# Kernel optimization log

Hardware: AMD Instinct MI355X
Metric: run time of the kernel (lower is better)

Reference implementation:

```python
import jax, jax.numpy as jnp
import numpy as np

HIDDEN = 1024
NUM_HEAD = 16
HEAD_DIM = HIDDEN // NUM_HEAD


def setup_inputs() -> dict:
    key = jax.random.key(0)
    ks = jax.random.split(key, 12)
    bs, seq = 4, 2048
    inp = {
        'srcQ': jax.random.normal(ks[0], (bs, seq, HIDDEN), jnp.float32),
        'srcK': jax.random.normal(ks[1], (bs, seq, HIDDEN), jnp.float32),
        'srcV': jax.random.normal(ks[2], (bs, seq, HIDDEN), jnp.float32),
        'mask': jnp.ones((bs, 1, 1, seq), jnp.int32),
        'Wq': jax.random.normal(ks[3], (HIDDEN, HIDDEN), jnp.float32) * 0.02,
        'bq': jnp.zeros((HIDDEN,), jnp.float32),
        'Wk': jax.random.normal(ks[4], (HIDDEN, HIDDEN), jnp.float32) * 0.02,
        'bk': jnp.zeros((HIDDEN,), jnp.float32),
        'Wv': jax.random.normal(ks[5], (HIDDEN, HIDDEN), jnp.float32) * 0.02,
        'bv': jnp.zeros((HIDDEN,), jnp.float32),
        'Wo': jax.random.normal(ks[6], (HIDDEN, HIDDEN), jnp.float32) * 0.02,
        'bo': jnp.zeros((HIDDEN,), jnp.float32),
    }
    return inp


def _split_heads(x):
    # [bs, seq, hidden] -> [bs, num_head, seq, head_dim]
    bs, seq, _ = x.shape
    return x.reshape(bs, seq, NUM_HEAD, HEAD_DIM).transpose(0, 2, 1, 3)


def reference(srcQ, srcK, srcV, mask, Wq, bq, Wk, bk, Wv, bv, Wo, bo):
    Q = _split_heads(srcQ @ Wq + bq)
    K = _split_heads(srcK @ Wk + bk)
    V = _split_heads(srcV @ Wv + bv)
    # NOTE: original module applies NO 1/sqrt(d) scaling (scale tensor unused)
    scores = jnp.einsum('bhqd,bhkd->bhqk', Q, K)
    scores = jnp.where(mask == 0, jnp.float32(-10000.0), scores)
    attn = jax.nn.softmax(scores, axis=-1)  # dropout is identity in eval
    out = jnp.einsum('bhqk,bhkd->bhqd', attn, V)
    bs, _, seq, _ = out.shape
    out = out.transpose(0, 2, 1, 3).reshape(bs, seq, HIDDEN)
    return out @ Wo + bo
```

## Files before the change

### kernel.cpp

```cpp
#include <hip/hip_runtime.h>

typedef short bf16x8 __attribute__((ext_vector_type(8)));
typedef short bf16x4 __attribute__((ext_vector_type(4)));
typedef float f32x4 __attribute__((ext_vector_type(4)));
typedef unsigned short ushort8 __attribute__((ext_vector_type(8)));
typedef unsigned short ushort4v __attribute__((ext_vector_type(4)));
typedef unsigned int uint4v __attribute__((ext_vector_type(4)));
typedef float float4v __attribute__((ext_vector_type(4)));

#define LOG2E 1.4426950408889634f
#define MASKED_VAL -14426.950408889634f

__device__ __forceinline__ unsigned short f2bf(float f) {
  unsigned u = __builtin_bit_cast(unsigned, f);
  u = u + 0x7fffu + ((u >> 16) & 1u);
  return (unsigned short)(u >> 16);
}

__device__ __forceinline__ unsigned pk2(float a, float b) {
  unsigned r;
  asm("v_cvt_pk_bf16_f32 %0, %1, %2" : "=v"(r) : "v"(a), "v"(b));
  return r;
}

__device__ __forceinline__ float exp2a(float x) {
  float r;
  asm("v_exp_f32 %0, %1" : "=v"(r) : "v"(x));
  return r;
}

__device__ __forceinline__ void gload16(const void* g, void* l) {
  __builtin_amdgcn_global_load_lds(
      (const __attribute__((address_space(1))) unsigned int*)g,
      (__attribute__((address_space(3))) unsigned int*)l, 16, 0, 0);
}

__global__ __launch_bounds__(256) void pack_w4(const float* __restrict__ W0,
                                               const float* __restrict__ W1,
                                               const float* __restrict__ W2,
                                               const float* __restrict__ W3,
                                               unsigned short* __restrict__ P) {
  __shared__ float tile[32][33];
  const int z = blockIdx.z;
  const float* W = (z == 0) ? W0 : (z == 1) ? W1 : (z == 2) ? W2 : W3;
  unsigned short* o = P + (size_t)z * (1 << 20);
  int bx = blockIdx.x * 32;
  int by = blockIdx.y * 32;
  int tx = threadIdx.x & 31;
  int ty = threadIdx.x >> 5;
#pragma unroll
  for (int j = 0; j < 32; j += 8)
    tile[ty + j][tx] = W[(size_t)(by + ty + j) * 1024 + bx + tx];
  __syncthreads();
  const int t = threadIdx.x;
  if (t < 128) {
    int col_l = t & 31, kg = t >> 5;
    int col = bx + col_l;
    ushort8 v;
#pragma unroll
    for (int j = 0; j < 8; ++j) v[j] = f2bf(tile[kg * 8 + j][col_l]);
    int bn = col >> 7, cl = col & 127;
    int wc = cl >> 6, n = (cl >> 4) & 3, lr = cl & 15;
    int ks = by >> 5;
    size_t off = (size_t)(bn * 32 + ks) * 4096 + (wc * 4 + n) * 512 + (kg * 16 + lr) * 8;
    *(ushort8*)&o[off] = v;
  }
}

__global__ __launch_bounds__(256, 3) void gemm_qkv(
    const float* __restrict__ srcQ, const float* __restrict__ srcK,
    const float* __restrict__ srcV, const unsigned short* __restrict__ Wp,
    const float* __restrict__ bq, const float* __restrict__ bk,
    const float* __restrict__ bv, unsigned short* __restrict__ Qb,
    unsigned short* __restrict__ Kb, unsigned short* __restrict__ Vt) {
  __shared__ __align__(16) unsigned short As[3][128 * 32];
  const int K = 1024, N = 1024;
  const int chunk = blockIdx.x >> 9;
  const int inner = blockIdx.x & 511;
  const int x = inner & 7, i = inner >> 3;
  const int bm = (x << 3) + (i >> 3);
  const int bn = i & 7;
  const float* Af = (chunk == 0) ? srcQ : (chunk == 1) ? srcK : srcV;
  const unsigned short* Pk = Wp + (size_t)chunk * (1 << 20);
  const float* bias = (chunk == 0) ? bq : (chunk == 1) ? bk : bv;
  const float scale = (chunk == 0) ? LOG2E : 1.0f;
  const int t = threadIdx.x;
  const int lane = t & 63, wid = t >> 6;
  const int wr = wid >> 1, wc = wid & 1;
  const int lr = lane & 15, lg = lane >> 4;
  f32x4 acc[4][4] = {};
  const size_t baseA = (size_t)(bm * 128) * K;
  const int c0 = t, c1 = t + 256;
  const size_t a0off = baseA + (size_t)(c0 >> 2) * K + (c0 & 3) * 8;
  const size_t a1off = baseA + (size_t)(c1 >> 2) * K + (c1 & 3) * 8;
  size_t bo[4];
#pragma unroll
  for (int n = 0; n < 4; ++n)
    bo[n] = (size_t)(bn * 32) * 4096 + (size_t)(wc * 4 + n) * 512 + (size_t)lane * 8;

  unsigned short* pA0 = &As[0][0];
  unsigned short* pA1 = &As[1][0];
  unsigned short* pA2 = &As[2][0];
  float4v fE[4], fO[4];
  bf16x8 bE[4], bO[4];

  auto loadA = [&](float4v* f, int ke) {
    f[0] = *(const float4v*)&Af[a0off + ke];
    f[1] = *(const float4v*)&Af[a0off + ke + 4];
    f[2] = *(const float4v*)&Af[a1off + ke];
    f[3] = *(const float4v*)&Af[a1off + ke + 4];
  };
  auto loadB = [&](bf16x8* b, int ks) {
#pragma unroll
    for (int n = 0; n < 4; ++n)
      b[n] = *(const bf16x8*)&Pk[bo[n] + (size_t)ks * 4096];
  };
  auto writeA = [&](const float4v* f, unsigned short* dst) {
    uint4v w0, w1;
    w0[0] = pk2(f[0][0], f[0][1]); w0[1] = pk2(f[0][2], f[0][3]);
    w0[2] = pk2(f[1][0], f[1][1]); w0[3] = pk2(f[1][2], f[1][3]);
    w1[0] = pk2(f[2][0], f[2][1]); w1[1] = pk2(f[2][2], f[2][3]);
    w1[2] = pk2(f[3][0], f[3][1]); w1[3] = pk2(f[3][2], f[3][3]);
    *(uint4v*)&dst[c0 * 8] = w0;
    *(uint4v*)&dst[c1 * 8] = w1;
  };
  auto compute = [&](const bf16x8* b) {
    bf16x8 a[4];
#pragma unroll
    for (int m = 0; m < 4; ++m)
      a[m] = *(const bf16x8*)&pA0[(wr * 64 + 16 * m + lr) * 32 + lg * 8];
    __builtin_amdgcn_s_setprio(1);
#pragma unroll
    for (int m = 0; m < 4; ++m)
#pragma unroll
      for (int n = 0; n < 4; ++n)
        acc[m][n] = __builtin_amdgcn_mfma_f32_16x16x32_bf16(a[m], b[n], acc[m][n], 0, 0, 0);
    __builtin_amdgcn_s_setprio(0);
  };
  auto rotate = [&]() {
    unsigned short* ta = pA0; pA0 = pA1; pA1 = pA2; pA2 = ta;
  };

  loadA(fE, 0);
  loadB(bE, 0);
  loadA(fO, 32);
  loadB(bO, 1);
  writeA(fE, pA0);
  asm volatile("s_waitcnt lgkmcnt(0)" ::: "memory");
  __builtin_amdgcn_s_barrier();

  for (int it = 0; it < 16; ++it) {
    const int t0 = 2 * it;
    if (it < 15) loadA(fE, 32 * (t0 + 2));
    compute(bE);
    if (t0 + 2 < 32) loadB(bE, t0 + 2);
    writeA(fO, pA1);
    asm volatile("s_waitcnt lgkmcnt(0)" ::: "memory");
    __builtin_amdgcn_sched_barrier(0);
    __builtin_amdgcn_s_barrier();
    rotate();
    if (it < 15) loadA(fO, 32 * (t0 + 3));
    compute(bO);
    if (t0 + 3 < 32) loadB(bO, t0 + 3);
    if (it < 15) {
      writeA(fE, pA1);
      asm volatile("s_waitcnt lgkmcnt(0)" ::: "memory");
      __builtin_amdgcn_sched_barrier(0);
      __builtin_amdgcn_s_barrier();
      rotate();
    }
  }

  const int rowb = bm * 128 + wr * 64;
  const int colb = bn * 128 + wc * 64;
  if (chunk == 2) {
    const int bidx = rowb >> 11;
    const int srow = rowb & 2047;
#pragma unroll
    for (int n = 0; n < 4; ++n) {
      int col = colb + 16 * n + lr;
      float bv_ = bias[col];
#pragma unroll
      for (int m = 0; m < 4; ++m) {
        int s0 = srow + 16 * m + 4 * lg;
        ushort4v u;
#pragma unroll
        for (int r = 0; r < 4; ++r) u[r] = f2bf(acc[m][n][r] + bv_);
        *(ushort4v*)&Vt[((size_t)(bidx * 1024 + col)) * 2048 + s0] = u;
      }
    }
  } else {
    unsigned short* C = (chunk == 0) ? Qb : Kb;
#pragma unroll
    for (int n = 0; n < 4; ++n) {
      int col = colb + 16 * n + lr;
      float bv_ = bias[col];
#pragma unroll
      for (int m = 0; m < 4; ++m) {
        int row0 = rowb + 16 * m + 4 * lg;
#pragma unroll
        for (int r = 0; r < 4; ++r)
          C[(size_t)(row0 + r) * N + col] = f2bf((acc[m][n][r] + bv_) * scale);
      }
    }
  }
}

__global__ __launch_bounds__(256, 3) void gemm_out(const unsigned short* __restrict__ A,
                                                   const unsigned short* __restrict__ Bp,
                                                   const float* __restrict__ bias,
                                                   float* __restrict__ C) {
  __shared__ __align__(16) unsigned short As[3][128 * 32];
  const int K = 1024, N = 1024;
  const int x = blockIdx.x & 7, i = blockIdx.x >> 3;
  const int bm = (x << 3) + (i >> 3);
  const int bn = i & 7;
  const int t = threadIdx.x;
  const int lane = t & 63, wid = t >> 6;
  const int wr = wid >> 1, wc = wid & 1;
  const int lr = lane & 15, lg = lane >> 4;
  f32x4 acc[4][4] = {};
  const size_t baseA = (size_t)(bm * 128) * K;
  const int c0 = t, c1 = t + 256;
  const size_t a0off = baseA + (size_t)(c0 >> 2) * K + (c0 & 3) * 8;
  const size_t a1off = baseA + (size_t)(c1 >> 2) * K + (c1 & 3) * 8;
  size_t bo[4];
#pragma unroll
  for (int n = 0; n < 4; ++n)
    bo[n] = (size_t)(bn * 32) * 4096 + (size_t)(wc * 4 + n) * 512 + (size_t)lane * 8;

  unsigned short* pA0 = &As[0][0];
  unsigned short* pA1 = &As[1][0];
  unsigned short* pA2 = &As[2][0];
  bf16x8 bE[4], bO[4];

  auto dmaA = [&](int ks, unsigned short* dA) {
    gload16(&A[a0off + 32 * ks], &dA[c0 * 8]);
    gload16(&A[a1off + 32 * ks], &dA[c1 * 8]);
  };
  auto loadB = [&](bf16x8* b, int ks) {
#pragma unroll
    for (int n = 0; n < 4; ++n)
      b[n] = *(const bf16x8*)&Bp[bo[n] + (size_t)ks * 4096];
  };
  auto compute = [&](const bf16x8* b) {
    bf16x8 a[4];
#pragma unroll
    for (int m = 0; m < 4; ++m)
      a[m] = *(const bf16x8*)&pA0[(wr * 64 + 16 * m + lr) * 32 + lg * 8];
    __builtin_amdgcn_s_setprio(1);
#pragma unroll
    for (int m = 0; m < 4; ++m)
#pragma unroll
      for (int n = 0; n < 4; ++n)
        acc[m][n] = __builtin_amdgcn_mfma_f32_16x16x32_bf16(a[m], b[n], acc[m][n], 0, 0, 0);
    __builtin_amdgcn_s_setprio(0);
  };
  auto rotate = [&]() {
    unsigned short* ta = pA0; pA0 = pA1; pA1 = pA2; pA2 = ta;
  };

  dmaA(0, pA0);
  dmaA(1, pA1);
  loadB(bE, 0);
  loadB(bO, 1);
  asm volatile("s_waitcnt vmcnt(10)" ::: "memory");
  __builtin_amdgcn_sched_barrier(0);
  __builtin_amdgcn_s_barrier();

  for (int it = 0; it < 16; ++it) {
    const int t0 = 2 * it;
    if (t0 + 2 < 32) dmaA(t0 + 2, pA2);
    compute(bE);
    if (t0 + 2 < 32) loadB(bE, t0 + 2);
    {
      if (t0 < 30) {
        asm volatile("s_waitcnt vmcnt(6)" ::: "memory");
      } else {
        asm volatile("s_waitcnt vmcnt(0)" ::: "memory");
      }
      __builtin_amdgcn_sched_barrier(0);
      __builtin_amdgcn_s_barrier();
      rotate();
    }
    if (t0 + 3 < 32) dmaA(t0 + 3, pA2);
    compute(bO);
    if (t0 + 3 < 32) loadB(bO, t0 + 3);
    if (it < 15) {
      if (t0 + 1 < 30) {
        asm volatile("s_waitcnt vmcnt(6)" ::: "memory");
      } else {
        asm volatile("s_waitcnt vmcnt(0)" ::: "memory");
      }
      __builtin_amdgcn_sched_barrier(0);
      __builtin_amdgcn_s_barrier();
      rotate();
    }
  }

  const int rowb = bm * 128 + wr * 64;
  const int colb = bn * 128 + wc * 64;
#pragma unroll
  for (int n = 0; n < 4; ++n) {
    int col = colb + 16 * n + lr;
    float bv = bias[col];
#pragma unroll
    for (int m = 0; m < 4; ++m) {
      int row0 = rowb + 16 * m + 4 * lg;
#pragma unroll
      for (int r = 0; r < 4; ++r)
        C[(size_t)(row0 + r) * N + col] = acc[m][n][r] + bv;
    }
  }
}

__global__ __launch_bounds__(512, 4) void attn_kernel(
    const unsigned short* __restrict__ Q, const unsigned short* __restrict__ K,
    const unsigned short* __restrict__ V, const int* __restrict__ mask,
    unsigned short* __restrict__ ctx) {
  __shared__ __align__(16) unsigned short pool[16384];
  __shared__ int s_any[8];
  unsigned short* Kbuf0 = pool;
  unsigned short* Kbuf1 = pool + 4096;
  unsigned short* Vbuf0 = pool + 8192;
  unsigned short* Vbuf1 = pool + 12288;
  const int g = blockIdx.x;
  const int bid = (g & 7) * 64 + (g >> 3);
  const int qb = bid & 7, h = (bid >> 3) & 15, b = bid >> 7;
  const int t = threadIdx.x;
  const int lane = t & 63, wid = t >> 6;
  const int lr = lane & 15, lg = lane >> 4;
  const size_t rowQ0 = (size_t)(b * 2048 + qb * 256);
  const int hcol = h * 64;
  const size_t vrow0 = (size_t)((b * 16 + h) * 64) * 2048;

  const int row_s = t >> 3, pos_s = t & 7;
  const size_t ksrc = (size_t)(b * 2048 + row_s) * 1024 + hcol + ((pos_s ^ (row_s & 7)) << 3);
  const size_t vsrc = vrow0 + (size_t)row_s * 2048 + ((pos_s ^ ((row_s >> 1) & 7)) << 3);
  const int ldso = t * 8;

#pragma unroll
  for (int i = 0; i < 4; ++i) {
    int ci = t + 512 * i;
    int row = ci >> 3, pos = ci & 7;
    gload16(&Q[(rowQ0 + row) * 1024 + hcol + ((pos ^ (row & 7)) << 3)], &pool[ci * 8]);
  }
  const int* mb = mask + b * 2048;
  int4 mv0 = *(const int4*)&mb[t * 4];
  int bad = (mv0.x == 0) | (mv0.y == 0) | (mv0.z == 0) | (mv0.w == 0);
  unsigned long long bb = __ballot(bad);
  if (lane == 0) s_any[wid] = (bb != 0ULL);
  __syncthreads();
  bf16x8 aq[2][2];
#pragma unroll
  for (int m = 0; m < 2; ++m)
#pragma unroll
    for (int kd = 0; kd < 2; ++kd) {
      int row = wid * 32 + 16 * m + lr;
      int ch = (4 * kd + lg) ^ (lr & 7);
      aq[m][kd] = *(const bf16x8*)&pool[row * 64 + ch * 8];
    }
  int anyi = 0;
#pragma unroll
  for (int w = 0; w < 8; ++w) anyi |= s_any[w];
  const bool anymask = anyi != 0;
  __syncthreads();
  gload16(&K[ksrc], &Kbuf0[ldso]);
  gload16(&V[vsrc], &Vbuf0[ldso]);
  __syncthreads();

  f32x4 o[2][4] = {};
  f32x4 ol[2] = {};
  const short oneb = 0x3F80;
  const bf16x8 ones8 = {oneb, oneb, oneb, oneb, oneb, oneb, oneb, oneb};
  const f32x4 zero4 = {0.f, 0.f, 0.f, 0.f};
  const int ch0 = (lg ^ (lr & 7)) * 8;
  const int ch1 = ((4 + lg) ^ (lr & 7)) * 8;
  const int sw = lr >> 1;

  for (int kb = 0; kb < 32; ++kb) {
    const int bi = kb & 1;
    const unsigned short* Kb_ = bi ? Kbuf1 : Kbuf0;
    const unsigned short* Vb_ = bi ? Vbuf1 : Vbuf0;
    unsigned short* Kn_ = bi ? Kbuf0 : Kbuf1;
    unsigned short* Vn_ = bi ? Vbuf0 : Vbuf1;
    if (kb + 1 < 32) {
      gload16(&K[ksrc + (size_t)(kb + 1) * 64 * 1024], &Kn_[ldso]);
      gload16(&V[vsrc + (size_t)(kb + 1) * 64], &Vn_[ldso]);
    }
    f32x4 s[2][4];
    __builtin_amdgcn_s_setprio(1);
#pragma unroll
    for (int n = 0; n < 4; ++n) {
      bf16x8 k0 = *(const bf16x8*)&Kb_[(16 * n + lr) * 64 + ch0];
      bf16x8 k1 = *(const bf16x8*)&Kb_[(16 * n + lr) * 64 + ch1];
      f32x4 t0 = __builtin_amdgcn_mfma_f32_16x16x32_bf16(k0, aq[0][0], zero4, 0, 0, 0);
      s[0][n] = __builtin_amdgcn_mfma_f32_16x16x32_bf16(k1, aq[0][1], t0, 0, 0, 0);
      f32x4 t1 = __builtin_amdgcn_mfma_f32_16x16x32_bf16(k0, aq[1][0], zero4, 0, 0, 0);
      s[1][n] = __builtin_amdgcn_mfma_f32_16x16x32_bf16(k1, aq[1][1], t1, 0, 0, 0);
    }
    __builtin_amdgcn_s_setprio(0);
    if (anymask) {
      const int* mrow = mb + kb * 64;
#pragma unroll
      for (int n = 0; n < 4; ++n) {
        int4 mv = *(const int4*)&mrow[16 * n + 4 * lg];
        int mm[4] = {mv.x, mv.y, mv.z, mv.w};
#pragma unroll
        for (int r = 0; r < 4; ++r)
          if (mm[r] == 0) { s[0][n][r] = MASKED_VAL; s[1][n][r] = MASKED_VAL; }
      }
    }
#pragma unroll
    for (int m = 0; m < 2; ++m)
#pragma unroll
      for (int n = 0; n < 4; ++n)
#pragma unroll
        for (int r = 0; r < 4; ++r) s[m][n][r] = exp2a(s[m][n][r]);
#pragma unroll
    for (int kk = 0; kk < 2; ++kk) {
      bf16x8 pf[2];
#pragma unroll
      for (int m = 0; m < 2; ++m) {
        uint4v u;
        u[0] = pk2(s[m][2 * kk][0], s[m][2 * kk][1]);
        u[1] = pk2(s[m][2 * kk][2], s[m][2 * kk][3]);
        u[2] = pk2(s[m][2 * kk + 1][0], s[m][2 * kk + 1][1]);
        u[3] = pk2(s[m][2 * kk + 1][2], s[m][2 * kk + 1][3]);
        pf[m] = __builtin_bit_cast(bf16x8, u);
      }
      __builtin_amdgcn_s_setprio(1);
      ol[0] = __builtin_amdgcn_mfma_f32_16x16x32_bf16(ones8, pf[0], ol[0], 0, 0, 0);
      ol[1] = __builtin_amdgcn_mfma_f32_16x16x32_bf16(ones8, pf[1], ol[1], 0, 0, 0);
      const int p0 = (4 * kk + (lg >> 1)) ^ sw;
      const int base0 = lr * 64 + p0 * 8 + (lg & 1) * 4;
      const int base1 = lr * 64 + (p0 ^ 2) * 8 + (lg & 1) * 4;
#pragma unroll
      for (int dn = 0; dn < 4; ++dn) {
        bf16x4 v0 = *(const bf16x4*)&Vb_[base0 + dn * 1024];
        bf16x4 v1 = *(const bf16x4*)&Vb_[base1 + dn * 1024];
        bf16x8 vb = __builtin_shufflevector(v0, v1, 0, 1, 2, 3, 4, 5, 6, 7);
#pragma unroll
        for (int m = 0; m < 2; ++m)
          o[m][dn] = __builtin_amdgcn_mfma_f32_16x16x32_bf16(vb, pf[m], o[m][dn], 0, 0, 0);
      }
      __builtin_amdgcn_s_setprio(0);
    }
    __syncthreads();
  }
#pragma unroll
  for (int m = 0; m < 2; ++m) {
    float inv = 1.f / ol[m][0];
    size_t q = rowQ0 + wid * 32 + 16 * m + lr;
#pragma unroll
    for (int dn = 0; dn < 4; ++dn) {
      ushort4v u;
#pragma unroll
      for (int r = 0; r < 4; ++r) u[r] = f2bf(o[m][dn][r] * inv);
      *(ushort4v*)&ctx[q * 1024 + hcol + 16 * dn + 4 * lg] = u;
    }
  }
}

extern "C" void kernel_launch(void* const* d_in, const int* in_sizes, int n_in,
                              void* d_out, int out_size, void* d_ws, size_t ws_size,
                              hipStream_t stream) {
  const float* srcQ = (const float*)d_in[0];
  const float* srcK = (const float*)d_in[1];
  const float* srcV = (const float*)d_in[2];
  const int*   mask = (const int*)d_in[3];
  const float* Wq = (const float*)d_in[4];
  const float* bq = (const float*)d_in[5];
  const float* Wk = (const float*)d_in[6];
  const float* bk = (const float*)d_in[7];
  const float* Wv = (const float*)d_in[8];
  const float* bv = (const float*)d_in[9];
  const float* Wo = (const float*)d_in[10];
  const float* bo = (const float*)d_in[11];
  float* out = (float*)d_out;

  char* ws = (char*)d_ws;
  unsigned short* ctx = (unsigned short*)(ws);
  unsigned short* Qb  = (unsigned short*)(ws + (size_t)(16 << 20));
  unsigned short* Kb  = (unsigned short*)(ws + (size_t)(32 << 20));
  unsigned short* Vt  = (unsigned short*)(ws + (size_t)(48 << 20));
  unsigned short* Wp  = (unsigned short*)(ws + (size_t)(64 << 20));

  pack_w4<<<dim3(32, 32, 4), 256, 0, stream>>>(Wq, Wk, Wv, Wo, Wp);

  gemm_qkv<<<1536, 256, 0, stream>>>(srcQ, srcK, srcV, Wp, bq, bk, bv, Qb, Kb, Vt);

  attn_kernel<<<512, 512, 0, stream>>>(Qb, Kb, Vt, mask, ctx);

  gemm_out<<<512, 256, 0, stream>>>(ctx, Wp + 3 * (1 << 20), bo, out);
}
```

Baseline: 170.5 us.

## Triple-buffer K/V tiles in attention with prefetch distance two

Changes the attention kernel's K/V shared-memory staging from double to triple buffering, issuing global-to-LDS loads two tiles ahead. It replaces the per-iteration __syncthreads with an explicit partial vmcnt wait plus s_barrier, so one tile's loads can stay in flight across the barrier. This raises LDS per block from 32KB to 48KB and drops the min-blocks launch bound, which may reduce occupancy.

```diff
diff --git a/kernel.cpp b/kernel.cpp
--- a/kernel.cpp
+++ b/kernel.cpp
@@ -314,16 +314,12 @@
   }
 }
 
-__global__ __launch_bounds__(512, 4) void attn_kernel(
+__global__ __launch_bounds__(512) void attn_kernel(
     const unsigned short* __restrict__ Q, const unsigned short* __restrict__ K,
     const unsigned short* __restrict__ V, const int* __restrict__ mask,
     unsigned short* __restrict__ ctx) {
-  __shared__ __align__(16) unsigned short pool[16384];
+  __shared__ __align__(16) unsigned short pool[24576];
   __shared__ int s_any[8];
-  unsigned short* Kbuf0 = pool;
-  unsigned short* Kbuf1 = pool + 4096;
-  unsigned short* Vbuf0 = pool + 8192;
-  unsigned short* Vbuf1 = pool + 12288;
   const int g = blockIdx.x;
   const int bid = (g & 7) * 64 + (g >> 3);
   const int qb = bid & 7, h = (bid >> 3) & 15, b = bid >> 7;
@@ -365,9 +361,22 @@
   for (int w = 0; w < 8; ++w) anyi |= s_any[w];
   const bool anymask = anyi != 0;
   __syncthreads();
-  gload16(&K[ksrc], &Kbuf0[ldso]);
-  gload16(&V[vsrc], &Vbuf0[ldso]);
-  __syncthreads();
+  unsigned short* Kbuf[3] = {pool, pool + 4096, pool + 8192};
+  unsigned short* Vbuf[3] = {pool + 12288, pool + 16384, pool + 20480};
+  gload16(&K[ksrc], &Kbuf[0][ldso]);
+  gload16(&V[vsrc], &Vbuf[0][ldso]);
+  gload16(&K[ksrc + 65536], &Kbuf[1][ldso]);
+  gload16(&V[vsrc + 64], &Vbuf[1][ldso]);
+  asm volatile("s_waitcnt vmcnt(2)" ::: "memory");
+  __builtin_amdgcn_sched_barrier(0);
+  __builtin_amdgcn_s_barrier();
+
+  unsigned short* kC = Kbuf[0];
+  unsigned short* kN = Kbuf[1];
+  unsigned short* kP = Kbuf[2];
+  unsigned short* vC = Vbuf[0];
+  unsigned short* vN = Vbuf[1];
+  unsigned short* vP = Vbuf[2];
 
   f32x4 o[2][4] = {};
   f32x4 ol[2] = {};
@@ -379,21 +388,16 @@
   const int sw = lr >> 1;
 
   for (int kb = 0; kb < 32; ++kb) {
-    const int bi = kb & 1;
-    const unsigned short* Kb_ = bi ? Kbuf1 : Kbuf0;
-    const unsigned short* Vb_ = bi ? Vbuf1 : Vbuf0;
-    unsigned short* Kn_ = bi ? Kbuf0 : Kbuf1;
-    unsigned short* Vn_ = bi ? Vbuf0 : Vbuf1;
-    if (kb + 1 < 32) {
-      gload16(&K[ksrc + (size_t)(kb + 1) * 64 * 1024], &Kn_[ldso]);
-      gload16(&V[vsrc + (size_t)(kb + 1) * 64], &Vn_[ldso]);
+    if (kb + 2 < 32) {
+      gload16(&K[ksrc + (size_t)(kb + 2) * 65536], &kP[ldso]);
+      gload16(&V[vsrc + (size_t)(kb + 2) * 64], &vP[ldso]);
     }
     f32x4 s[2][4];
     __builtin_amdgcn_s_setprio(1);
 #pragma unroll
     for (int n = 0; n < 4; ++n) {
-      bf16x8 k0 = *(const bf16x8*)&Kb_[(16 * n + lr) * 64 + ch0];
-      bf16x8 k1 = *(const bf16x8*)&Kb_[(16 * n + lr) * 64 + ch1];
+      bf16x8 k0 = *(const bf16x8*)&kC[(16 * n + lr) * 64 + ch0];
+      bf16x8 k1 = *(const bf16x8*)&kC[(16 * n + lr) * 64 + ch1];
       f32x4 t0 = __builtin_amdgcn_mfma_f32_16x16x32_bf16(k0, aq[0][0], zero4, 0, 0, 0);
       s[0][n] = __builtin_amdgcn_mfma_f32_16x16x32_bf16(k1, aq[0][1], t0, 0, 0, 0);
       f32x4 t1 = __builtin_amdgcn_mfma_f32_16x16x32_bf16(k0, aq[1][0], zero4, 0, 0, 0);
@@ -437,8 +441,8 @@
       const int base1 = lr * 64 + (p0 ^ 2) * 8 + (lg & 1) * 4;
 #pragma unroll
       for (int dn = 0; dn < 4; ++dn) {
-        bf16x4 v0 = *(const bf16x4*)&Vb_[base0 + dn * 1024];
-        bf16x4 v1 = *(const bf16x4*)&Vb_[base1 + dn * 1024];
+        bf16x4 v0 = *(const bf16x4*)&vC[base0 + dn * 1024];
+        bf16x4 v1 = *(const bf16x4*)&vC[base1 + dn * 1024];
         bf16x8 vb = __builtin_shufflevector(v0, v1, 0, 1, 2, 3, 4, 5, 6, 7);
 #pragma unroll
         for (int m = 0; m < 2; ++m)
@@ -446,7 +450,17 @@
       }
       __builtin_amdgcn_s_setprio(0);
     }
-    __syncthreads();
+    if (kb + 1 < 32) {
+      if (kb + 2 < 32) {
+        asm volatile("s_waitcnt vmcnt(2)" ::: "memory");
+      } else {
+        asm volatile("s_waitcnt vmcnt(0)" ::: "memory");
+      }
+      __builtin_amdgcn_sched_barrier(0);
+      __builtin_amdgcn_s_barrier();
+      unsigned short* tk = kC; kC = kN; kN = kP; kP = tk;
+      unsigned short* tv = vC; vC = vN; vN = vP; vP = tv;
+    }
   }
 #pragma unroll
   for (int m = 0; m < 2; ++m) {
```

Result: slower. 193.6 us (+13.5%).
